# Kernel optimization log

Measured on AMD Instinct MI355X. Metric: run time of the kernel, lower is better.

## Reference

```python
import jax, jax.numpy as jnp
import numpy as np

B, N, N_IN, N_H = 8192, 16, 512, 256
NEG_ROUND = 1
MARGIN = 0.5
EPS = 1e-6  # torch F.pairwise_distance default eps


def setup_inputs() -> dict:
    key = jax.random.key(0)
    k0, k1, k2, k3 = jax.random.split(key, 4)
    seq1 = jax.random.normal(k0, (B, N, N_IN), dtype=jnp.float32)
    adj = jax.random.uniform(k1, (B, N, N), dtype=jnp.float32)
    # GCN linear (bias=False), xavier_uniform on [n_h, n_in] == same bound for [n_in, n_h]
    gx = float(np.sqrt(6.0 / (N_IN + N_H)))
    W_gcn = jax.random.uniform(k2, (N_IN, N_H), dtype=jnp.float32, minval=-gx, maxval=gx)
    b_gcn = jnp.zeros((N_H,), dtype=jnp.float32)  # Simple_GCN self.bias, init 0
    prelu_a = jnp.asarray(0.25, dtype=jnp.float32)  # nn.PReLU default
    bx = float(np.sqrt(6.0 / (N_H + N_H)))
    W_bil = jax.random.uniform(k3, (N_H, N_H), dtype=jnp.float32, minval=-bx, maxval=bx)
    b_bil = jnp.zeros((), dtype=jnp.float32)
    return {"seq1": seq1, "adj": adj, "W_gcn": W_gcn, "b_gcn": b_gcn,
            "prelu_a": prelu_a, "W_bil": W_bil, "b_bil": b_bil}


def reference(seq1, adj, W_gcn, b_gcn, prelu_a, W_bil, b_bil):
    # Simple_GCN: linear -> adjacency aggregate -> bias -> PReLU
    seq_fts = jnp.einsum('bnf,fh->bnh', seq1, W_gcn)           # [B,N,n_h]
    h1 = jnp.einsum('bnm,bmh->bnh', adj, seq_fts) + b_gcn      # bmm(adj, seq_fts)+bias
    h1 = jnp.where(h1 >= 0, h1, prelu_a * h1)                  # PReLU

    # avg readout over context nodes; last node is the target
    c = jnp.mean(h1[:, :-1, :], axis=1)                        # [B,n_h]
    h_mv = h1[:, -1, :]                                        # [B,n_h]

    def bilinear(x1, x2):  # nn.Bilinear(n_h, n_h, 1)
        return jnp.einsum('bi,ij,bj->b', x1, W_bil, x2)[:, None] + b_bil  # [B,1]

    scs = [bilinear(h_mv, c)]
    c_mi = c
    for _ in range(NEG_ROUND):  # fixed small loop, mirrors torch shift
        c_mi = jnp.concatenate([c_mi[-2:-1, :], c_mi[:-1, :]], axis=0)
        scs.append(bilinear(h_mv, c_mi))

    pos_dis = jnp.linalg.norm(h_mv - c + EPS, axis=-1)         # F.pairwise_distance
    neg_dis = jnp.linalg.norm(h_mv - c_mi + EPS, axis=-1)

    logits = jnp.concatenate(scs, axis=0)                      # [(1+NEG)*B, 1]
    # MarginRankingLoss(margin, reduction='none') with y=-1:
    # max(0, -y*(x1-x2)+margin) = max(0, (pos-neg)+margin)
    loss2 = jnp.maximum(0.0, (pos_dis - neg_dis) + MARGIN)     # [B]
    return (logits, loss2)
```

## Files before the change

kernel.cpp:

```cpp
#include <hip/hip_runtime.h>
#include <stdint.h>

typedef float f32x4 __attribute__((ext_vector_type(4)));
typedef __bf16 bfrag __attribute__((ext_vector_type(8)));
typedef unsigned short us4 __attribute__((ext_vector_type(4)));

__device__ __forceinline__ unsigned short f2bf(float f) {
  unsigned u = __float_as_uint(f);
  u += 0x7fff + ((u >> 16) & 1);
  return (unsigned short)(u >> 16);
}
__device__ __forceinline__ float bf2f(unsigned short s) {
  return __uint_as_float(((unsigned)s) << 16);
}

typedef __attribute__((address_space(3))) void lds_vp;
typedef __attribute__((address_space(1))) void gl_vp;
__device__ __forceinline__ void gload16(const void* g, void* l) {
  __builtin_amdgcn_global_load_lds((const gl_vp*)g, (lds_vp*)l, 16, 0, 0);
}

__global__ __launch_bounds__(256)
void conv_w_k(const float* __restrict__ Wg, const float* __restrict__ Wb,
              unsigned short* __restrict__ WgT, unsigned short* __restrict__ WbT) {
  int i = blockIdx.x * 256 + threadIdx.x;
  if (i < 512 * 256) { int k = i >> 8, c = i & 255; WgT[c * 512 + k] = f2bf(Wg[i]); }
  if (i < 256 * 256) { int k = i >> 8, c = i & 255; WbT[c * 256 + k] = f2bf(Wb[i]); }
}

__device__ __forceinline__ void stage1(const float* __restrict__ A,
                                       const unsigned short* __restrict__ Bt,
                                       char* buf, int wg, int kc, int t) {
#pragma unroll
  for (int i = 0; i < 2; i++) {
    int c = i * 512 + t;
    int row = c >> 3, s = c & 7;
    int sp = s ^ (((row & 3) << 1) | ((row >> 2) & 1));
    gload16(A + (size_t)(wg * 128 + row) * 512 + kc * 32 + sp * 4, buf + c * 16);
  }
#pragma unroll
  for (int i = 0; i < 2; i++) {
    int c = i * 512 + t;
    int col = c >> 2, s = c & 3;
    int sp = s ^ ((col ^ (col >> 2)) & 3);
    gload16(Bt + (size_t)col * 512 + kc * 32 + sp * 8, buf + 16384 + c * 16);
  }
}

__global__ __launch_bounds__(512, 4)
void fused1_k(const float* __restrict__ A, const unsigned short* __restrict__ Bt,
              const float* __restrict__ adj, const float* __restrict__ b_gcn,
              const float* __restrict__ prelu_a,
              float* __restrict__ Cout, float* __restrict__ Hmv) {
  __shared__ char sm[65536];
  const int t = threadIdx.x;
  const int lane = t & 63;
  const int wid = t >> 6;
  const int wm = wid >> 2, wn = wid & 3;
  const int lrow = lane & 15, lgrp = lane >> 4;
  const int wg = blockIdx.x;

  f32x4 acc[4][4];
#pragma unroll
  for (int m = 0; m < 4; m++)
#pragma unroll
    for (int n = 0; n < 4; n++) acc[m][n] = (f32x4)0.0f;

  stage1(A, Bt, sm, wg, 0, t);

  for (int kc = 0; kc < 16; ++kc) {
    char* cur = sm + (kc & 1) * 32768;
    if (kc + 1 < 16) {
      stage1(A, Bt, sm + ((kc + 1) & 1) * 32768, wg, kc + 1, t);
      asm volatile("s_waitcnt vmcnt(4)" ::: "memory");
    } else {
      asm volatile("s_waitcnt vmcnt(0)" ::: "memory");
    }
    __builtin_amdgcn_s_barrier();
    asm volatile("" ::: "memory");

    bfrag bf[4];
#pragma unroll
    for (int n = 0; n < 4; n++) {
      int bcol = wn * 64 + n * 16 + lrow;
      int sB = (bcol ^ (bcol >> 2)) & 3;
      bf[n] = *(const bfrag*)(cur + 16384 + bcol * 64 + ((lgrp ^ sB) << 4));
    }
#pragma unroll
    for (int m = 0; m < 4; m++) {
      int arow = wm * 64 + m * 16 + lrow;
      int sw = ((arow & 3) << 1) | ((arow >> 2) & 1);
      f32x4 lo = *(const f32x4*)(cur + arow * 128 + (((lgrp * 2) ^ sw) << 4));
      f32x4 hi = *(const f32x4*)(cur + arow * 128 + (((lgrp * 2 + 1) ^ sw) << 4));
      bfrag am;
      am[0] = (__bf16)lo.x; am[1] = (__bf16)lo.y; am[2] = (__bf16)lo.z; am[3] = (__bf16)lo.w;
      am[4] = (__bf16)hi.x; am[5] = (__bf16)hi.y; am[6] = (__bf16)hi.z; am[7] = (__bf16)hi.w;
#pragma unroll
      for (int n = 0; n < 4; n++)
        acc[m][n] = __builtin_amdgcn_mfma_f32_16x16x32_bf16(am, bf[n], acc[m][n], 0, 0, 0);
    }
    __builtin_amdgcn_s_barrier();
    asm volatile("" ::: "memory");
  }

  unsigned short* sf = (unsigned short*)sm;
#pragma unroll
  for (int m = 0; m < 4; m++) {
    int row = wm * 64 + m * 16 + lgrp * 4;
#pragma unroll
    for (int n = 0; n < 4; n++) {
      int col = wn * 64 + n * 16 + lrow;
#pragma unroll
      for (int rr = 0; rr < 4; rr++)
        sf[(row + rr) * 256 + col] = f2bf(acc[m][n][rr]);
    }
  }
  __builtin_amdgcn_s_barrier();
  asm volatile("" ::: "memory");

  const float pa = prelu_a[0];
  const f32x4 bg = *(const f32x4*)(b_gcn + lane * 4);
  f32x4 sfr[16];
#pragma unroll
  for (int mm = 0; mm < 16; mm++) {
    us4 q = *(const us4*)(sf + (wid * 16 + mm) * 256 + lane * 4);
    f32x4 v;
    v.x = bf2f(q.x); v.y = bf2f(q.y); v.z = bf2f(q.z); v.w = bf2f(q.w);
    sfr[mm] = v;
  }
  const int b = wg * 8 + wid;
  const float* adjb = adj + (size_t)b * 256;
  f32x4 cacc = (f32x4)0.0f;
  f32x4 hmv = (f32x4)0.0f;
#pragma unroll
  for (int n = 0; n < 16; n++) {
    f32x4 a4 = (f32x4)0.0f;
#pragma unroll
    for (int m = 0; m < 16; m++) a4 += adjb[n * 16 + m] * sfr[m];
    a4 += bg;
    f32x4 hv;
    hv.x = a4.x >= 0.f ? a4.x : pa * a4.x;
    hv.y = a4.y >= 0.f ? a4.y : pa * a4.y;
    hv.z = a4.z >= 0.f ? a4.z : pa * a4.z;
    hv.w = a4.w >= 0.f ? a4.w : pa * a4.w;
    if (n < 15) cacc += hv; else hmv = hv;
  }
  cacc *= (1.0f / 15.0f);
  *(f32x4*)(Cout + (size_t)b * 256 + lane * 4) = cacc;
  *(f32x4*)(Hmv + (size_t)b * 256 + lane * 4) = hmv;
}

__device__ __forceinline__ void stage2(const float* __restrict__ A,
                                       const unsigned short* __restrict__ Bt,
                                       char* buf, int wg, int kc, int t) {
  {
    int c = t;
    int row = c >> 3, s = c & 7;
    int sp = s ^ (((row & 3) << 1) | ((row >> 2) & 1));
    gload16(A + (size_t)(wg * 64 + row) * 256 + kc * 32 + sp * 4, buf + c * 16);
  }
#pragma unroll
  for (int i = 0; i < 2; i++) {
    int c = i * 512 + t;
    int col = c >> 2, s = c & 3;
    int sp = s ^ ((col ^ (col >> 2)) & 3);
    gload16(Bt + (size_t)col * 256 + kc * 32 + sp * 8, buf + 8192 + c * 16);
  }
}

__global__ __launch_bounds__(512)
void fused2_k(const float* __restrict__ A, const unsigned short* __restrict__ Bt,
              const float* __restrict__ C, const float* __restrict__ Hmv,
              const float* __restrict__ b_bil, float* __restrict__ out) {
  __shared__ char sm[65536];
  const int t = threadIdx.x;
  const int lane = t & 63;
  const int wid = t >> 6;
  const int wm = wid >> 2, wn = wid & 3;
  const int lrow = lane & 15, lgrp = lane >> 4;
  const int wg = blockIdx.x;

  f32x4 acc[2][4];
#pragma unroll
  for (int m = 0; m < 2; m++)
#pragma unroll
    for (int n = 0; n < 4; n++) acc[m][n] = (f32x4)0.0f;

  stage2(A, Bt, sm, wg, 0, t);

  for (int kc = 0; kc < 8; ++kc) {
    char* cur = sm + (kc & 1) * 24576;
    if (kc + 1 < 8) {
      stage2(A, Bt, sm + ((kc + 1) & 1) * 24576, wg, kc + 1, t);
      asm volatile("s_waitcnt vmcnt(3)" ::: "memory");
    } else {
      asm volatile("s_waitcnt vmcnt(0)" ::: "memory");
    }
    __builtin_amdgcn_s_barrier();
    asm volatile("" ::: "memory");

    bfrag bf[4];
#pragma unroll
    for (int n = 0; n < 4; n++) {
      int bcol = wn * 64 + n * 16 + lrow;
      int sB = (bcol ^ (bcol >> 2)) & 3;
      bf[n] = *(const bfrag*)(cur + 8192 + bcol * 64 + ((lgrp ^ sB) << 4));
    }
#pragma unroll
    for (int m = 0; m < 2; m++) {
      int arow = wm * 32 + m * 16 + lrow;
      int sw = ((arow & 3) << 1) | ((arow >> 2) & 1);
      f32x4 lo = *(const f32x4*)(cur + arow * 128 + (((lgrp * 2) ^ sw) << 4));
      f32x4 hi = *(const f32x4*)(cur + arow * 128 + (((lgrp * 2 + 1) ^ sw) << 4));
      bfrag am;
      am[0] = (__bf16)lo.x; am[1] = (__bf16)lo.y; am[2] = (__bf16)lo.z; am[3] = (__bf16)lo.w;
      am[4] = (__bf16)hi.x; am[5] = (__bf16)hi.y; am[6] = (__bf16)hi.z; am[7] = (__bf16)hi.w;
#pragma unroll
      for (int n = 0; n < 4; n++)
        acc[m][n] = __builtin_amdgcn_mfma_f32_16x16x32_bf16(am, bf[n], acc[m][n], 0, 0, 0);
    }
    __builtin_amdgcn_s_barrier();
    asm volatile("" ::: "memory");
  }

  float* sf = (float*)sm;
#pragma unroll
  for (int m = 0; m < 2; m++) {
    int row = wm * 32 + m * 16 + lgrp * 4;
#pragma unroll
    for (int n = 0; n < 4; n++) {
      int col = wn * 64 + n * 16 + lrow;
#pragma unroll
      for (int rr = 0; rr < 4; rr++)
        sf[(row + rr) * 256 + col] = acc[m][n][rr];
    }
  }
  __builtin_amdgcn_s_barrier();
  asm volatile("" ::: "memory");

  const float bb = b_bil[0];
#pragma unroll
  for (int r = 0; r < 8; ++r) {
    const int row = wid * 8 + r;
    const int b = wg * 64 + row;
    const int bp = (b == 0) ? 8190 : (b - 1);
    f32x4 tv = *(const f32x4*)(sf + row * 256 + lane * 4);
    f32x4 cv = *(const f32x4*)(C + (size_t)b * 256 + lane * 4);
    f32x4 cp = *(const f32x4*)(C + (size_t)bp * 256 + lane * 4);
    f32x4 hv = *(const f32x4*)(Hmv + (size_t)b * 256 + lane * 4);
    f32x4 d0 = hv - cv + 1e-6f;
    f32x4 d1 = hv - cp + 1e-6f;
    float s0 = tv.x * cv.x + tv.y * cv.y + tv.z * cv.z + tv.w * cv.w;
    float s1 = tv.x * cp.x + tv.y * cp.y + tv.z * cp.z + tv.w * cp.w;
    float p = d0.x * d0.x + d0.y * d0.y + d0.z * d0.z + d0.w * d0.w;
    float q = d1.x * d1.x + d1.y * d1.y + d1.z * d1.z + d1.w * d1.w;
#pragma unroll
    for (int m = 1; m < 64; m <<= 1) {
      s0 += __shfl_xor(s0, m, 64);
      s1 += __shfl_xor(s1, m, 64);
      p  += __shfl_xor(p, m, 64);
      q  += __shfl_xor(q, m, 64);
    }
    if (lane == 0) {
      out[b] = s0 + bb;
      out[8192 + b] = s1 + bb;
      out[16384 + b] = fmaxf(0.0f, sqrtf(p) - sqrtf(q) + 0.5f);
    }
  }
}

extern "C" void kernel_launch(void* const* d_in, const int* in_sizes, int n_in,
                              void* d_out, int out_size, void* d_ws, size_t ws_size,
                              hipStream_t stream) {
  (void)in_sizes; (void)n_in; (void)out_size; (void)ws_size;
  const float* seq1 = (const float*)d_in[0];
  const float* adj  = (const float*)d_in[1];
  const float* Wg   = (const float*)d_in[2];
  const float* bg   = (const float*)d_in[3];
  const float* pa   = (const float*)d_in[4];
  const float* Wb   = (const float*)d_in[5];
  const float* bb   = (const float*)d_in[6];
  float* out = (float*)d_out;
  char* ws = (char*)d_ws;

  unsigned short* WgT = (unsigned short*)(ws);
  unsigned short* WbT = (unsigned short*)(ws + 262144);
  float* C   = (float*)(ws + 524288);
  float* HMV = (float*)(ws + 524288 + 8388608);

  hipLaunchKernelGGL(conv_w_k, dim3(512), dim3(256), 0, stream, Wg, Wb, WgT, WbT);
  hipLaunchKernelGGL(fused1_k, dim3(1024), dim3(512), 0, stream,
                     seq1, WgT, adj, bg, pa, C, HMV);
  hipLaunchKernelGGL(fused2_k, dim3(128), dim3(512), 0, stream,
                     HMV, WbT, C, HMV, bb, out);
}
```

Measured before the change: 100.3 us.

## Make GCN GEMM kernel persistent over four tiles with wider K chunks

fused1_k now launches 256 blocks that each loop over four 128-row tiles. It uses 128KB of dynamic LDS with a 64-wide K chunk and an 8-way XOR swizzle, and prefetches the next tile's first chunk during the last chunk of the current one. The aim is to cut block launch and pipeline fill overhead and to halve barriers per K. fused2_k is re-tiled to 32 rows per block, giving 256 blocks for better CU occupancy. The trade-off is one block per CU for fused1, so latency hiding relies entirely on the intra-block double buffer.

Result: slower. 104.8 us (+4.5%).

```diff
diff --git a/kernel.cpp b/kernel.cpp
--- a/kernel.cpp
+++ b/kernel.cpp
@@ -30,29 +30,29 @@
 
 __device__ __forceinline__ void stage1(const float* __restrict__ A,
                                        const unsigned short* __restrict__ Bt,
-                                       char* buf, int wg, int kc, int t) {
-#pragma unroll
-  for (int i = 0; i < 2; i++) {
+                                       char* buf, int tile, int kc, int t) {
+#pragma unroll
+  for (int i = 0; i < 4; i++) {
     int c = i * 512 + t;
-    int row = c >> 3, s = c & 7;
-    int sp = s ^ (((row & 3) << 1) | ((row >> 2) & 1));
-    gload16(A + (size_t)(wg * 128 + row) * 512 + kc * 32 + sp * 4, buf + c * 16);
-  }
-#pragma unroll
-  for (int i = 0; i < 2; i++) {
+    int row = c >> 4, s = c & 15;
+    int sp = s ^ (row & 7);
+    gload16(A + (size_t)(tile * 128 + row) * 512 + kc * 64 + sp * 4, buf + c * 16);
+  }
+#pragma unroll
+  for (int i = 0; i < 4; i++) {
     int c = i * 512 + t;
-    int col = c >> 2, s = c & 3;
-    int sp = s ^ ((col ^ (col >> 2)) & 3);
-    gload16(Bt + (size_t)col * 512 + kc * 32 + sp * 8, buf + 16384 + c * 16);
-  }
-}
-
-__global__ __launch_bounds__(512, 4)
+    int col = c >> 3, s = c & 7;
+    int sp = s ^ (col & 7);
+    gload16(Bt + (size_t)col * 512 + kc * 64 + sp * 8, buf + 32768 + c * 16);
+  }
+}
+
+__global__ __launch_bounds__(512)
 void fused1_k(const float* __restrict__ A, const unsigned short* __restrict__ Bt,
               const float* __restrict__ adj, const float* __restrict__ b_gcn,
               const float* __restrict__ prelu_a,
               float* __restrict__ Cout, float* __restrict__ Hmv) {
-  __shared__ char sm[65536];
+  extern __shared__ __align__(16) char sm[];
   const int t = threadIdx.x;
   const int lane = t & 63;
   const int wid = t >> 6;
@@ -60,19 +60,152 @@
   const int lrow = lane & 15, lgrp = lane >> 4;
   const int wg = blockIdx.x;
 
-  f32x4 acc[4][4];
-#pragma unroll
-  for (int m = 0; m < 4; m++)
-#pragma unroll
-    for (int n = 0; n < 4; n++) acc[m][n] = (f32x4)0.0f;
-
-  stage1(A, Bt, sm, wg, 0, t);
-
-  for (int kc = 0; kc < 16; ++kc) {
-    char* cur = sm + (kc & 1) * 32768;
-    if (kc + 1 < 16) {
-      stage1(A, Bt, sm + ((kc + 1) & 1) * 32768, wg, kc + 1, t);
-      asm volatile("s_waitcnt vmcnt(4)" ::: "memory");
+  const float pa = prelu_a[0];
+  const f32x4 bg = *(const f32x4*)(b_gcn + lane * 4);
+
+  stage1(A, Bt, sm, wg * 4, 0, t);
+
+  for (int mt = 0; mt < 4; ++mt) {
+    const int tile = wg * 4 + mt;
+    f32x4 acc[4][4];
+#pragma unroll
+    for (int m = 0; m < 4; m++)
+#pragma unroll
+      for (int n = 0; n < 4; n++) acc[m][n] = (f32x4)0.0f;
+
+    for (int kc = 0; kc < 8; ++kc) {
+      char* cur = sm + (kc & 1) * 65536;
+      if (!(mt == 3 && kc == 7)) {
+        int nt = (kc < 7) ? tile : tile + 1;
+        int nk = (kc < 7) ? kc + 1 : 0;
+        stage1(A, Bt, sm + ((kc + 1) & 1) * 65536, nt, nk, t);
+        asm volatile("s_waitcnt vmcnt(8)" ::: "memory");
+      } else {
+        asm volatile("s_waitcnt vmcnt(0)" ::: "memory");
+      }
+      __builtin_amdgcn_s_barrier();
+      asm volatile("" ::: "memory");
+
+#pragma unroll
+      for (int kk = 0; kk < 2; kk++) {
+        bfrag bfv[4];
+#pragma unroll
+        for (int n = 0; n < 4; n++) {
+          int bcol = wn * 64 + n * 16 + lrow;
+          int gs = (kk * 4 + lgrp) ^ (bcol & 7);
+          bfv[n] = *(const bfrag*)(cur + 32768 + bcol * 128 + (gs << 4));
+        }
+#pragma unroll
+        for (int m = 0; m < 4; m++) {
+          int arow = wm * 64 + m * 16 + lrow;
+          int s0 = (kk * 8 + lgrp * 2) ^ (arow & 7);
+          int s1 = (kk * 8 + lgrp * 2 + 1) ^ (arow & 7);
+          f32x4 lo = *(const f32x4*)(cur + arow * 256 + (s0 << 4));
+          f32x4 hi = *(const f32x4*)(cur + arow * 256 + (s1 << 4));
+          bfrag am;
+          am[0] = (__bf16)lo.x; am[1] = (__bf16)lo.y; am[2] = (__bf16)lo.z; am[3] = (__bf16)lo.w;
+          am[4] = (__bf16)hi.x; am[5] = (__bf16)hi.y; am[6] = (__bf16)hi.z; am[7] = (__bf16)hi.w;
+#pragma unroll
+          for (int n = 0; n < 4; n++)
+            acc[m][n] = __builtin_amdgcn_mfma_f32_16x16x32_bf16(am, bfv[n], acc[m][n], 0, 0, 0);
+        }
+      }
+      __builtin_amdgcn_s_barrier();
+      asm volatile("" ::: "memory");
+    }
+
+    unsigned short* sf = (unsigned short*)(sm + 65536);
+#pragma unroll
+    for (int m = 0; m < 4; m++) {
+      int row = wm * 64 + m * 16 + lgrp * 4;
+#pragma unroll
+      for (int n = 0; n < 4; n++) {
+        int col = wn * 64 + n * 16 + lrow;
+#pragma unroll
+        for (int rr = 0; rr < 4; rr++)
+          sf[(row + rr) * 256 + col] = f2bf(acc[m][n][rr]);
+      }
+    }
+    asm volatile("s_waitcnt lgkmcnt(0)" ::: "memory");
+    __builtin_amdgcn_s_barrier();
+    asm volatile("" ::: "memory");
+
+    f32x4 sfr[16];
+#pragma unroll
+    for (int mm = 0; mm < 16; mm++) {
+      us4 q = *(const us4*)(sf + (wid * 16 + mm) * 256 + lane * 4);
+      f32x4 v;
+      v.x = bf2f(q.x); v.y = bf2f(q.y); v.z = bf2f(q.z); v.w = bf2f(q.w);
+      sfr[mm] = v;
+    }
+    const int b = tile * 8 + wid;
+    const float* adjb = adj + (size_t)b * 256;
+    f32x4 cacc = (f32x4)0.0f;
+    f32x4 hmv = (f32x4)0.0f;
+#pragma unroll
+    for (int n = 0; n < 16; n++) {
+      f32x4 a4 = (f32x4)0.0f;
+#pragma unroll
+      for (int m = 0; m < 16; m++) a4 += adjb[n * 16 + m] * sfr[m];
+      a4 += bg;
+      f32x4 hv;
+      hv.x = a4.x >= 0.f ? a4.x : pa * a4.x;
+      hv.y = a4.y >= 0.f ? a4.y : pa * a4.y;
+      hv.z = a4.z >= 0.f ? a4.z : pa * a4.z;
+      hv.w = a4.w >= 0.f ? a4.w : pa * a4.w;
+      if (n < 15) cacc += hv; else hmv = hv;
+    }
+    cacc *= (1.0f / 15.0f);
+    *(f32x4*)(Cout + (size_t)b * 256 + lane * 4) = cacc;
+    *(f32x4*)(Hmv + (size_t)b * 256 + lane * 4) = hmv;
+
+    asm volatile("s_waitcnt lgkmcnt(0)" ::: "memory");
+    __builtin_amdgcn_s_barrier();
+    asm volatile("" ::: "memory");
+  }
+}
+
+__device__ __forceinline__ void stage2(const float* __restrict__ A,
+                                       const unsigned short* __restrict__ Bt,
+                                       char* buf, int wg, int kc, int t) {
+  {
+    int c = t & 255;
+    int row = c >> 3, s = c & 7;
+    int sp = s ^ (((row & 3) << 1) | ((row >> 2) & 1));
+    gload16(A + (size_t)(wg * 32 + row) * 256 + kc * 32 + sp * 4, buf + c * 16);
+  }
+#pragma unroll
+  for (int i = 0; i < 2; i++) {
+    int c = i * 512 + t;
+    int col = c >> 2, s = c & 3;
+    int sp = s ^ ((col ^ (col >> 2)) & 3);
+    gload16(Bt + (size_t)col * 256 + kc * 32 + sp * 8, buf + 4096 + c * 16);
+  }
+}
+
+__global__ __launch_bounds__(512)
+void fused2_k(const float* __restrict__ A, const unsigned short* __restrict__ Bt,
+              const float* __restrict__ C, const float* __restrict__ Hmv,
+              const float* __restrict__ b_bil, float* __restrict__ out) {
+  __shared__ __align__(16) char sm2[40960];
+  const int t = threadIdx.x;
+  const int lane = t & 63;
+  const int wid = t >> 6;
+  const int wm = wid >> 2, wn = wid & 3;
+  const int lrow = lane & 15, lgrp = lane >> 4;
+  const int wg = blockIdx.x;
+
+  f32x4 acc[4];
+#pragma unroll
+  for (int n = 0; n < 4; n++) acc[n] = (f32x4)0.0f;
+
+  stage2(A, Bt, sm2, wg, 0, t);
+
+  for (int kc = 0; kc < 8; ++kc) {
+    char* cur = sm2 + (kc & 1) * 20480;
+    if (kc + 1 < 8) {
+      stage2(A, Bt, sm2 + ((kc + 1) & 1) * 20480, wg, kc + 1, t);
+      asm volatile("s_waitcnt vmcnt(3)" ::: "memory");
     } else {
       asm volatile("s_waitcnt vmcnt(0)" ::: "memory");
     }
@@ -84,11 +217,10 @@
     for (int n = 0; n < 4; n++) {
       int bcol = wn * 64 + n * 16 + lrow;
       int sB = (bcol ^ (bcol >> 2)) & 3;
-      bf[n] = *(const bfrag*)(cur + 16384 + bcol * 64 + ((lgrp ^ sB) << 4));
-    }
-#pragma unroll
-    for (int m = 0; m < 4; m++) {
-      int arow = wm * 64 + m * 16 + lrow;
+      bf[n] = *(const bfrag*)(cur + 4096 + bcol * 64 + ((lgrp ^ sB) << 4));
+    }
+    {
+      int arow = wm * 16 + lrow;
       int sw = ((arow & 3) << 1) | ((arow >> 2) & 1);
       f32x4 lo = *(const f32x4*)(cur + arow * 128 + (((lgrp * 2) ^ sw) << 4));
       f32x4 hi = *(const f32x4*)(cur + arow * 128 + (((lgrp * 2 + 1) ^ sw) << 4));
@@ -97,152 +229,32 @@
       am[4] = (__bf16)hi.x; am[5] = (__bf16)hi.y; am[6] = (__bf16)hi.z; am[7] = (__bf16)hi.w;
 #pragma unroll
       for (int n = 0; n < 4; n++)
-        acc[m][n] = __builtin_amdgcn_mfma_f32_16x16x32_bf16(am, bf[n], acc[m][n], 0, 0, 0);
+        acc[n] = __builtin_amdgcn_mfma_f32_16x16x32_bf16(am, bf[n], acc[n], 0, 0, 0);
     }
     __builtin_amdgcn_s_barrier();
     asm volatile("" ::: "memory");
   }
 
-  unsigned short* sf = (unsigned short*)sm;
-#pragma unroll
-  for (int m = 0; m < 4; m++) {
-    int row = wm * 64 + m * 16 + lgrp * 4;
+  float* sf = (float*)sm2;
+  {
+    int row = wm * 16 + lgrp * 4;
 #pragma unroll
     for (int n = 0; n < 4; n++) {
       int col = wn * 64 + n * 16 + lrow;
 #pragma unroll
       for (int rr = 0; rr < 4; rr++)
-        sf[(row + rr) * 256 + col] = f2bf(acc[m][n][rr]);
-    }
-  }
+        sf[(row + rr) * 256 + col] = acc[n][rr];
+    }
+  }
+  asm volatile("s_waitcnt lgkmcnt(0)" ::: "memory");
   __builtin_amdgcn_s_barrier();
   asm volatile("" ::: "memory");
 
-  const float pa = prelu_a[0];
-  const f32x4 bg = *(const f32x4*)(b_gcn + lane * 4);
-  f32x4 sfr[16];
-#pragma unroll
-  for (int mm = 0; mm < 16; mm++) {
-    us4 q = *(const us4*)(sf + (wid * 16 + mm) * 256 + lane * 4);
-    f32x4 v;
-    v.x = bf2f(q.x); v.y = bf2f(q.y); v.z = bf2f(q.z); v.w = bf2f(q.w);
-    sfr[mm] = v;
-  }
-  const int b = wg * 8 + wid;
-  const float* adjb = adj + (size_t)b * 256;
-  f32x4 cacc = (f32x4)0.0f;
-  f32x4 hmv = (f32x4)0.0f;
-#pragma unroll
-  for (int n = 0; n < 16; n++) {
-    f32x4 a4 = (f32x4)0.0f;
-#pragma unroll
-    for (int m = 0; m < 16; m++) a4 += adjb[n * 16 + m] * sfr[m];
-    a4 += bg;
-    f32x4 hv;
-    hv.x = a4.x >= 0.f ? a4.x : pa * a4.x;
-    hv.y = a4.y >= 0.f ? a4.y : pa * a4.y;
-    hv.z = a4.z >= 0.f ? a4.z : pa * a4.z;
-    hv.w = a4.w >= 0.f ? a4.w : pa * a4.w;
-    if (n < 15) cacc += hv; else hmv = hv;
-  }
-  cacc *= (1.0f / 15.0f);
-  *(f32x4*)(Cout + (size_t)b * 256 + lane * 4) = cacc;
-  *(f32x4*)(Hmv + (size_t)b * 256 + lane * 4) = hmv;
-}
-
-__device__ __forceinline__ void stage2(const float* __restrict__ A,
-                                       const unsigned short* __restrict__ Bt,
-                                       char* buf, int wg, int kc, int t) {
-  {
-    int c = t;
-    int row = c >> 3, s = c & 7;
-    int sp = s ^ (((row & 3) << 1) | ((row >> 2) & 1));
-    gload16(A + (size_t)(wg * 64 + row) * 256 + kc * 32 + sp * 4, buf + c * 16);
-  }
-#pragma unroll
-  for (int i = 0; i < 2; i++) {
-    int c = i * 512 + t;
-    int col = c >> 2, s = c & 3;
-    int sp = s ^ ((col ^ (col >> 2)) & 3);
-    gload16(Bt + (size_t)col * 256 + kc * 32 + sp * 8, buf + 8192 + c * 16);
-  }
-}
-
-__global__ __launch_bounds__(512)
-void fused2_k(const float* __restrict__ A, const unsigned short* __restrict__ Bt,
-              const float* __restrict__ C, const float* __restrict__ Hmv,
-              const float* __restrict__ b_bil, float* __restrict__ out) {
-  __shared__ char sm[65536];
-  const int t = threadIdx.x;
-  const int lane = t & 63;
-  const int wid = t >> 6;
-  const int wm = wid >> 2, wn = wid & 3;
-  const int lrow = lane & 15, lgrp = lane >> 4;
-  const int wg = blockIdx.x;
-
-  f32x4 acc[2][4];
-#pragma unroll
-  for (int m = 0; m < 2; m++)
-#pragma unroll
-    for (int n = 0; n < 4; n++) acc[m][n] = (f32x4)0.0f;
-
-  stage2(A, Bt, sm, wg, 0, t);
-
-  for (int kc = 0; kc < 8; ++kc) {
-    char* cur = sm + (kc & 1) * 24576;
-    if (kc + 1 < 8) {
-      stage2(A, Bt, sm + ((kc + 1) & 1) * 24576, wg, kc + 1, t);
-      asm volatile("s_waitcnt vmcnt(3)" ::: "memory");
-    } else {
-      asm volatile("s_waitcnt vmcnt(0)" ::: "memory");
-    }
-    __builtin_amdgcn_s_barrier();
-    asm volatile("" ::: "memory");
-
-    bfrag bf[4];
-#pragma unroll
-    for (int n = 0; n < 4; n++) {
-      int bcol = wn * 64 + n * 16 + lrow;
-      int sB = (bcol ^ (bcol >> 2)) & 3;
-      bf[n] = *(const bfrag*)(cur + 8192 + bcol * 64 + ((lgrp ^ sB) << 4));
-    }
-#pragma unroll
-    for (int m = 0; m < 2; m++) {
-      int arow = wm * 32 + m * 16 + lrow;
-      int sw = ((arow & 3) << 1) | ((arow >> 2) & 1);
-      f32x4 lo = *(const f32x4*)(cur + arow * 128 + (((lgrp * 2) ^ sw) << 4));
-      f32x4 hi = *(const f32x4*)(cur + arow * 128 + (((lgrp * 2 + 1) ^ sw) << 4));
-      bfrag am;
-      am[0] = (__bf16)lo.x; am[1] = (__bf16)lo.y; am[2] = (__bf16)lo.z; am[3] = (__bf16)lo.w;
-      am[4] = (__bf16)hi.x; am[5] = (__bf16)hi.y; am[6] = (__bf16)hi.z; am[7] = (__bf16)hi.w;
-#pragma unroll
-      for (int n = 0; n < 4; n++)
-        acc[m][n] = __builtin_amdgcn_mfma_f32_16x16x32_bf16(am, bf[n], acc[m][n], 0, 0, 0);
-    }
-    __builtin_amdgcn_s_barrier();
-    asm volatile("" ::: "memory");
-  }
-
-  float* sf = (float*)sm;
-#pragma unroll
-  for (int m = 0; m < 2; m++) {
-    int row = wm * 32 + m * 16 + lgrp * 4;
-#pragma unroll
-    for (int n = 0; n < 4; n++) {
-      int col = wn * 64 + n * 16 + lrow;
-#pragma unroll
-      for (int rr = 0; rr < 4; rr++)
-        sf[(row + rr) * 256 + col] = acc[m][n][rr];
-    }
-  }
-  __builtin_amdgcn_s_barrier();
-  asm volatile("" ::: "memory");
-
   const float bb = b_bil[0];
 #pragma unroll
-  for (int r = 0; r < 8; ++r) {
-    const int row = wid * 8 + r;
-    const int b = wg * 64 + row;
+  for (int r = 0; r < 4; ++r) {
+    const int row = wid * 4 + r;
+    const int b = wg * 32 + row;
     const int bp = (b == 0) ? 8190 : (b - 1);
     f32x4 tv = *(const f32x4*)(sf + row * 256 + lane * 4);
     f32x4 cv = *(const f32x4*)(C + (size_t)b * 256 + lane * 4);
@@ -288,9 +300,12 @@
   float* C   = (float*)(ws + 524288);
   float* HMV = (float*)(ws + 524288 + 8388608);
 
+  (void)hipFuncSetAttribute((const void*)fused1_k,
+                            hipFuncAttributeMaxDynamicSharedMemorySize, 131072);
+
   hipLaunchKernelGGL(conv_w_k, dim3(512), dim3(256), 0, stream, Wg, Wb, WgT, WbT);
-  hipLaunchKernelGGL(fused1_k, dim3(1024), dim3(512), 0, stream,
+  hipLaunchKernelGGL(fused1_k, dim3(256), dim3(512), 131072, stream,
                      seq1, WgT, adj, bg, pa, C, HMV);
-  hipLaunchKernelGGL(fused2_k, dim3(128), dim3(512), 0, stream,
+  hipLaunchKernelGGL(fused2_k, dim3(256), dim3(512), 0, stream,
                      HMV, WbT, C, HMV, bb, out);
 }
```
